# Performance work log

Measured on AMD Instinct MI355X. Metric: run time of the kernel, lower is better.

## Reference

```python
import jax, jax.numpy as jnp
import numpy as np

NQ = 12  # qubits == features of M
# (op, theta_offset_or_control, wire_or_target) mirroring TTN_node_forward
CIRCUIT = [
    ("u3", 0, 0), ("u3", 3, 1), ("cx", 0, 1),
    ("u3", 6, 2), ("u3", 9, 3), ("cx", 3, 2),
    ("u3", 12, 4), ("u3", 15, 5), ("cx", 4, 5),
    ("u3", 18, 6), ("u3", 21, 7), ("cx", 7, 6),
    ("u3", 24, 8), ("u3", 27, 9), ("cx", 8, 9),
    ("u3", 30, 10), ("u3", 33, 11), ("cx", 11, 10),
    ("u3", 36, 1), ("u3", 39, 2), ("cx", 1, 2),
    ("u3", 42, 5), ("u3", 45, 6), ("cx", 6, 5),
    ("u3", 48, 9), ("u3", 51, 10), ("cx", 10, 9),
    ("u3", 54, 2), ("u3", 57, 5), ("cx", 2, 5),
    ("u3", 60, 5), ("u3", 63, 9), ("cx", 5, 9),
    ("u3", 66, 4),
]

def _u3(theta, phi, lam):
    ct, st = jnp.cos(theta / 2), jnp.sin(theta / 2)
    r0 = jnp.stack([ct + 0j, -jnp.exp(1j * lam) * st])
    r1 = jnp.stack([jnp.exp(1j * phi) * st, jnp.exp(1j * (phi + lam)) * ct])
    return jnp.stack([r0, r1])  # [2,2] complex64

def _apply_1q(state, U, w):
    # state: (N, 2, ..., 2) with 12 qubit axes; contract U into axis w+1
    out = jnp.tensordot(U, state, axes=((1,), (w + 1,)))
    return jnp.moveaxis(out, 0, w + 1)

def _apply_cnot(state, c, t):
    c_ax, t_ax = c + 1, t + 1
    s0 = jnp.take(state, 0, axis=c_ax)
    s1 = jnp.take(state, 1, axis=c_ax)
    t_adj = t_ax - 1 if t_ax > c_ax else t_ax
    s1 = jnp.flip(s1, axis=t_adj)  # X on target (size-2 axis flip)
    return jnp.stack([s0, s1], axis=c_ax)

def _simulate(M, theta):
    # M: (N, 12) angles; product state from RY(M[:, q]) |0>
    N = M.shape[0]
    state = jnp.ones((N,), dtype=jnp.complex64)
    for q in range(NQ):
        qv = jnp.stack([jnp.cos(M[:, q] / 2), jnp.sin(M[:, q] / 2)], axis=-1)
        qv = qv.astype(jnp.complex64).reshape((N,) + (1,) * q + (2,))
        state = state[..., None] * qv  # (N, 2^(q+1) as axes)
    for op, a, b in CIRCUIT:
        if op == "u3":
            state = _apply_1q(state, _u3(theta[a], theta[a + 1], theta[a + 2]), b)
        else:
            state = _apply_cnot(state, a, b)
    p = jnp.real(state) ** 2 + jnp.imag(state) ** 2  # probabilities
    sum_axes = tuple(ax for ax in range(1, NQ + 1) if ax != 10)  # keep wire 9
    pz = p.sum(axis=sum_axes)  # (N, 2)
    return pz[:, 0] - pz[:, 1]  # <Z_9>

def setup_inputs() -> dict:
    key = jax.random.key(0)
    k1, k2, k3, k4, k5 = jax.random.split(key, 5)
    N, E = 2048, 4096
    X = jax.random.normal(k1, (N, 4), dtype=jnp.float32)
    e = jax.random.uniform(k2, (E,), dtype=jnp.float32)
    Ri = jax.random.uniform(k3, (N, E), dtype=jnp.float32)
    Ro = jax.random.uniform(k4, (N, E), dtype=jnp.float32)
    theta_learn = jax.random.uniform(k5, (69,), dtype=jnp.float32,
                                     minval=0.0, maxval=2.0 * np.pi)
    return {"X": X, "e": e, "Ri": Ri, "Ro": Ro, "theta_learn": theta_learn}

def reference(X, e, Ri, Ro, theta_learn):
    bo = jnp.einsum('ne,nd->ed', Ro, X)          # Ro^T X
    bi = jnp.einsum('ne,nd->ed', Ri, X)          # Ri^T X
    mi = jnp.einsum('ne,ed->nd', Ri * e[None, :], bo)
    mo = jnp.einsum('ne,ed->nd', Ro * e[None, :], bi)
    M = jnp.concatenate([mi, mo, X], axis=1)     # (N, 12)
    z = _simulate(M, theta_learn)
    return jnp.pi * (1.0 - z)                    # 2*pi*(1 - <Z>)/2
```

## Files before the change

kernel.cpp:

```cpp
#include <hip/hip_runtime.h>
#include <math.h>

#define N_SAMPLES 2048
#define E_EDGES   4096
#define NSPLIT    64
#define SPB       4

__global__ __launch_bounds__(256) void k_partial(const float* __restrict__ Ri,
                                                 const float* __restrict__ Ro,
                                                 const float* __restrict__ X,
                                                 float* __restrict__ pbo,
                                                 float* __restrict__ pbi) {
    __shared__ float comb[128][33];

    const int ec   = blockIdx.x;
    const int ns   = blockIdx.y;
    const int t    = threadIdx.x;
    const int col  = t & 127;
    const int half = t >> 7;
    const int v    = ec * 128 + col;

    const float4* Ri4 = reinterpret_cast<const float4*>(Ri);
    const float4* Ro4 = reinterpret_cast<const float4*>(Ro);
    const float4* X4  = reinterpret_cast<const float4*>(X);

    float abo[4][4], abi[4][4];
#pragma unroll
    for (int c = 0; c < 4; ++c)
#pragma unroll
        for (int d = 0; d < 4; ++d) { abo[c][d] = 0.f; abi[c][d] = 0.f; }

    const int n0 = ns * 32 + half * 16;
#pragma unroll 4
    for (int n = n0; n < n0 + 16; ++n) {
        float4 xv = X4[n];
        float4 ro = Ro4[(size_t)n * 1024 + v];
        float4 ri = Ri4[(size_t)n * 1024 + v];
        float xs[4]  = {xv.x, xv.y, xv.z, xv.w};
        float ros[4] = {ro.x, ro.y, ro.z, ro.w};
        float ris[4] = {ri.x, ri.y, ri.z, ri.w};
#pragma unroll
        for (int c = 0; c < 4; ++c)
#pragma unroll
            for (int d = 0; d < 4; ++d) {
                abo[c][d] += ros[c] * xs[d];
                abi[c][d] += ris[c] * xs[d];
            }
    }

    if (half) {
#pragma unroll
        for (int c = 0; c < 4; ++c)
#pragma unroll
            for (int d = 0; d < 4; ++d) {
                comb[col][c * 4 + d]      = abo[c][d];
                comb[col][16 + c * 4 + d] = abi[c][d];
            }
    }
    __syncthreads();
    if (!half) {
        float4* pbo4 = reinterpret_cast<float4*>(pbo);
        float4* pbi4 = reinterpret_cast<float4*>(pbi);
#pragma unroll
        for (int c = 0; c < 4; ++c) {
#pragma unroll
            for (int d = 0; d < 4; ++d) {
                abo[c][d] += comb[col][c * 4 + d];
                abi[c][d] += comb[col][16 + c * 4 + d];
            }
            size_t idx = (size_t)ns * E_EDGES + 4 * (size_t)v + c;
            pbo4[idx] = make_float4(abo[c][0], abo[c][1], abo[c][2], abo[c][3]);
            pbi4[idx] = make_float4(abi[c][0], abi[c][1], abi[c][2], abi[c][3]);
        }
    }
}

__global__ __launch_bounds__(256) void k_reduce(const float* __restrict__ pbo,
                                                const float* __restrict__ pbi,
                                                const float* __restrict__ ev,
                                                float* __restrict__ boT,
                                                float* __restrict__ biT) {
    const int gid = blockIdx.x * 256 + threadIdx.x;
    const int q   = gid & 3;
    const int e   = (gid >> 2) & 4095;
    const int mat = gid >> 14;
    const float4* src = reinterpret_cast<const float4*>(mat ? pbi : pbo);
    float*        dst = mat ? biT : boT;

    float s0 = 0.f, s1 = 0.f, s2 = 0.f, s3 = 0.f;
#pragma unroll 4
    for (int ns = q * 16; ns < q * 16 + 16; ++ns) {
        float4 a = src[(size_t)ns * E_EDGES + e];
        s0 += a.x; s1 += a.y; s2 += a.z; s3 += a.w;
    }
    s0 += __shfl_xor(s0, 1); s0 += __shfl_xor(s0, 2);
    s1 += __shfl_xor(s1, 1); s1 += __shfl_xor(s1, 2);
    s2 += __shfl_xor(s2, 1); s2 += __shfl_xor(s2, 2);
    s3 += __shfl_xor(s3, 1); s3 += __shfl_xor(s3, 2);
    if (q == 0) {
        const float w = ev[e];
        dst[0 * E_EDGES + e] = w * s0;
        dst[1 * E_EDGES + e] = w * s1;
        dst[2 * E_EDGES + e] = w * s2;
        dst[3 * E_EDGES + e] = w * s3;
    }
}

__global__ __launch_bounds__(256) void k_sim(const float* __restrict__ Ri,
                                             const float* __restrict__ Ro,
                                             const float* __restrict__ X,
                                             const float* __restrict__ th,
                                             const float* __restrict__ boT,
                                             const float* __restrict__ biT,
                                             float* __restrict__ out) {
    __shared__ float  redM[4][SPB][8];
    __shared__ float  R[22][9];
    __shared__ float  sM[SPB][12], cM[SPB][12];

    const int n0   = blockIdx.x * SPB;
    const int t    = threadIdx.x;
    const int lane = t & 63;
    const int wv   = t >> 6;

    if (t < 22) {
        float T = th[3 * t], P = th[3 * t + 1], L = th[3 * t + 2];
        float st, ct, sp, cp, sl, cl;
        sincosf(T, &st, &ct);
        sincosf(P, &sp, &cp);
        sincosf(L, &sl, &cl);
        R[t][0] =  cp * ct * cl - sp * sl;
        R[t][1] = -cp * ct * sl - sp * cl;
        R[t][2] =  cp * st;
        R[t][3] =  sp * ct * cl + cp * sl;
        R[t][4] = -sp * ct * sl + cp * cl;
        R[t][5] =  sp * st;
        R[t][6] = -st * cl;
        R[t][7] =  st * sl;
        R[t][8] =  ct;
    }

    float accf[SPB][8];
#pragma unroll
    for (int s = 0; s < SPB; ++s)
#pragma unroll
        for (int j = 0; j < 8; ++j) accf[s][j] = 0.f;

    const float4* Ri4s[SPB];
    const float4* Ro4s[SPB];
#pragma unroll
    for (int s = 0; s < SPB; ++s) {
        Ri4s[s] = reinterpret_cast<const float4*>(Ri + (size_t)(n0 + s) * E_EDGES);
        Ro4s[s] = reinterpret_cast<const float4*>(Ro + (size_t)(n0 + s) * E_EDGES);
    }
    const float4* BO0 = reinterpret_cast<const float4*>(boT);
    const float4* BO1 = reinterpret_cast<const float4*>(boT + E_EDGES);
    const float4* BO2 = reinterpret_cast<const float4*>(boT + 2 * E_EDGES);
    const float4* BO3 = reinterpret_cast<const float4*>(boT + 3 * E_EDGES);
    const float4* BI0 = reinterpret_cast<const float4*>(biT);
    const float4* BI1 = reinterpret_cast<const float4*>(biT + E_EDGES);
    const float4* BI2 = reinterpret_cast<const float4*>(biT + 2 * E_EDGES);
    const float4* BI3 = reinterpret_cast<const float4*>(biT + 3 * E_EDGES);

#pragma unroll
    for (int k = 0; k < 4; ++k) {
        const int v = t + 256 * k;
        const float4 o0 = BO0[v], o1 = BO1[v], o2 = BO2[v], o3 = BO3[v];
        const float4 i0 = BI0[v], i1 = BI1[v], i2 = BI2[v], i3 = BI3[v];
#pragma unroll
        for (int s = 0; s < SPB; ++s) {
            const float4 ri = Ri4s[s][v];
            const float4 ro = Ro4s[s][v];
            accf[s][0] += ri.x * o0.x + ri.y * o0.y + ri.z * o0.z + ri.w * o0.w;
            accf[s][1] += ri.x * o1.x + ri.y * o1.y + ri.z * o1.z + ri.w * o1.w;
            accf[s][2] += ri.x * o2.x + ri.y * o2.y + ri.z * o2.z + ri.w * o2.w;
            accf[s][3] += ri.x * o3.x + ri.y * o3.y + ri.z * o3.z + ri.w * o3.w;
            accf[s][4] += ro.x * i0.x + ro.y * i0.y + ro.z * i0.z + ro.w * i0.w;
            accf[s][5] += ro.x * i1.x + ro.y * i1.y + ro.z * i1.z + ro.w * i1.w;
            accf[s][6] += ro.x * i2.x + ro.y * i2.y + ro.z * i2.z + ro.w * i2.w;
            accf[s][7] += ro.x * i3.x + ro.y * i3.y + ro.z * i3.z + ro.w * i3.w;
        }
    }

#pragma unroll
    for (int off = 32; off >= 1; off >>= 1)
#pragma unroll
        for (int s = 0; s < SPB; ++s)
#pragma unroll
            for (int j = 0; j < 8; ++j)
                accf[s][j] += __shfl_xor(accf[s][j], off);
    if (lane == 0)
#pragma unroll
        for (int s = 0; s < SPB; ++s)
#pragma unroll
            for (int j = 0; j < 8; ++j) redM[wv][s][j] = accf[s][j];
    __syncthreads();

    if (t < 12 * SPB) {
        const int s = t / 12, w = t % 12;
        double Mw = (w < 8)
            ? ((double)redM[0][s][w] + (double)redM[1][s][w] +
               (double)redM[2][s][w] + (double)redM[3][s][w])
            : (double)X[(n0 + s) * 4 + (w - 8)];
        double sv, cv;
        sincos(Mw, &sv, &cv);
        sM[s][w] = (float)sv; cM[s][w] = (float)cv;
    }
    __syncthreads();

    if (t < SPB) {
        const float* sMv = sM[t];
        const float* cMv = cM[t];
        auto iz = [&](int g) -> float {
            return R[g][6] * sMv[g] + R[g][8] * cMv[g];
        };
        auto ivec = [&](int g, float& x, float& y, float& z) {
            x = R[g][0] * sMv[g] + R[g][2] * cMv[g];
            y = R[g][3] * sMv[g] + R[g][5] * cMv[g];
            z = R[g][6] * sMv[g] + R[g][8] * cMv[g];
        };
        auto rot = [&](int g, float& x, float& y, float& z) {
            float nx = R[g][0] * x + R[g][1] * y + R[g][2] * z;
            float ny = R[g][3] * x + R[g][4] * y + R[g][5] * z;
            float nz = R[g][6] * x + R[g][7] * y + R[g][8] * z;
            x = nx; y = ny; z = nz;
        };

        const float z0  = iz(0),  z3  = iz(3), z4 = iz(4);
        const float z7  = iz(7),  z8  = iz(8), z11 = iz(11);

        float x1, y1, z1;  ivec(1, x1, y1, z1);
        y1 *= z0;  z1 *= z0;          rot(12, x1, y1, z1);

        float x2, y2, z2;  ivec(2, x2, y2, z2);
        y2 *= z3;  z2 *= z3;          rot(13, x2, y2, z2);
        y2 *= z1;  z2 *= z1;          rot(18, x2, y2, z2);

        float x6, y6, z6;  ivec(6, x6, y6, z6);
        y6 *= z7;  z6 *= z7;          rot(15, x6, y6, z6);

        float x5, y5, z5;  ivec(5, x5, y5, z5);
        y5 *= z4;  z5 *= z4;          rot(14, x5, y5, z5);
        y5 *= z6;  z5 *= z6;          rot(19, x5, y5, z5);
        y5 *= z2;  z5 *= z2;          rot(20, x5, y5, z5);

        float xA, yA, zA;  ivec(10, xA, yA, zA);
        yA *= z11; zA *= z11;         rot(17, xA, yA, zA);

        float x9, y9, z9;  ivec(9, x9, y9, z9);
        y9 *= z8;  z9 *= z8;          rot(16, x9, y9, z9);
        y9 *= zA;  z9 *= zA;          rot(21, x9, y9, z9);
        z9 *= z5;

        out[n0 + t] = (float)(3.14159265358979323846 * (1.0 - (double)z9));
    }
}

extern "C" void kernel_launch(void* const* d_in, const int* in_sizes, int n_in,
                              void* d_out, int out_size, void* d_ws, size_t ws_size,
                              hipStream_t stream) {
    (void)in_sizes; (void)n_in; (void)out_size; (void)ws_size;
    const float* X  = (const float*)d_in[0];
    const float* ev = (const float*)d_in[1];
    const float* Ri = (const float*)d_in[2];
    const float* Ro = (const float*)d_in[3];
    const float* th = (const float*)d_in[4];
    float* out = (float*)d_out;

    float* pbo = (float*)d_ws;
    float* pbi = pbo + (size_t)NSPLIT * E_EDGES * 4;
    float* boT = pbi + (size_t)NSPLIT * E_EDGES * 4;
    float* biT = boT + (size_t)4 * E_EDGES;

    hipLaunchKernelGGL(k_partial, dim3(8, NSPLIT), dim3(256), 0, stream,
                       Ri, Ro, X, pbo, pbi);
    hipLaunchKernelGGL(k_reduce, dim3(128), dim3(256), 0, stream,
                       pbo, pbi, ev, boT, biT);
    hipLaunchKernelGGL(k_sim, dim3(N_SAMPLES / SPB), dim3(256), 0, stream,
                       Ri, Ro, X, th, boT, biT, out);
}
```

Before: 38.36 us.

## Double split count for partial Gram sums and use nontemporal partial stores

Splits the N dimension of the Ro^T X / Ri^T X partial products into 128 chunks instead of 64, doubling the k_partial grid to 1024 blocks to raise occupancy on the bandwidth-bound streaming pass. The reduce kernel is widened to 8 lanes per edge with an extra shuffle step and twice the blocks. Partial results are written and read with nontemporal hints to avoid polluting cache. In exchange, the partial buffers double in size, adding write and read traffic in the reduce stage.

```diff
diff --git a/kernel.cpp b/kernel.cpp
--- a/kernel.cpp
+++ b/kernel.cpp
@@ -3,8 +3,18 @@
 
 #define N_SAMPLES 2048
 #define E_EDGES   4096
-#define NSPLIT    64
+#define NSPLIT    128
 #define SPB       4
+
+typedef float f32x4 __attribute__((ext_vector_type(4)));
+
+__device__ __forceinline__ void nt_store4(float* p, float a, float b, float c, float d) {
+    f32x4 v = { a, b, c, d };
+    __builtin_nontemporal_store(v, (f32x4*)p);
+}
+__device__ __forceinline__ f32x4 nt_load4(const float* p) {
+    return __builtin_nontemporal_load((const f32x4*)p);
+}
 
 __global__ __launch_bounds__(256) void k_partial(const float* __restrict__ Ri,
                                                  const float* __restrict__ Ro,
@@ -30,9 +40,9 @@
 #pragma unroll
         for (int d = 0; d < 4; ++d) { abo[c][d] = 0.f; abi[c][d] = 0.f; }
 
-    const int n0 = ns * 32 + half * 16;
-#pragma unroll 4
-    for (int n = n0; n < n0 + 16; ++n) {
+    const int n0 = ns * 16 + half * 8;
+#pragma unroll
+    for (int n = n0; n < n0 + 8; ++n) {
         float4 xv = X4[n];
         float4 ro = Ro4[(size_t)n * 1024 + v];
         float4 ri = Ri4[(size_t)n * 1024 + v];
@@ -59,8 +69,6 @@
     }
     __syncthreads();
     if (!half) {
-        float4* pbo4 = reinterpret_cast<float4*>(pbo);
-        float4* pbi4 = reinterpret_cast<float4*>(pbi);
 #pragma unroll
         for (int c = 0; c < 4; ++c) {
 #pragma unroll
@@ -68,9 +76,9 @@
                 abo[c][d] += comb[col][c * 4 + d];
                 abi[c][d] += comb[col][16 + c * 4 + d];
             }
-            size_t idx = (size_t)ns * E_EDGES + 4 * (size_t)v + c;
-            pbo4[idx] = make_float4(abo[c][0], abo[c][1], abo[c][2], abo[c][3]);
-            pbi4[idx] = make_float4(abi[c][0], abi[c][1], abi[c][2], abi[c][3]);
+            size_t idx = 4 * ((size_t)ns * E_EDGES + 4 * (size_t)v + c);
+            nt_store4(pbo + idx, abo[c][0], abo[c][1], abo[c][2], abo[c][3]);
+            nt_store4(pbi + idx, abi[c][0], abi[c][1], abi[c][2], abi[c][3]);
         }
     }
 }
@@ -81,22 +89,22 @@
                                                 float* __restrict__ boT,
                                                 float* __restrict__ biT) {
     const int gid = blockIdx.x * 256 + threadIdx.x;
-    const int q   = gid & 3;
-    const int e   = (gid >> 2) & 4095;
-    const int mat = gid >> 14;
-    const float4* src = reinterpret_cast<const float4*>(mat ? pbi : pbo);
-    float*        dst = mat ? biT : boT;
+    const int q   = gid & 7;
+    const int e   = (gid >> 3) & 4095;
+    const int mat = gid >> 15;
+    const float* src = mat ? pbi : pbo;
+    float*       dst = mat ? biT : boT;
 
     float s0 = 0.f, s1 = 0.f, s2 = 0.f, s3 = 0.f;
 #pragma unroll 4
     for (int ns = q * 16; ns < q * 16 + 16; ++ns) {
-        float4 a = src[(size_t)ns * E_EDGES + e];
+        f32x4 a = nt_load4(src + 4 * ((size_t)ns * E_EDGES + e));
         s0 += a.x; s1 += a.y; s2 += a.z; s3 += a.w;
     }
-    s0 += __shfl_xor(s0, 1); s0 += __shfl_xor(s0, 2);
-    s1 += __shfl_xor(s1, 1); s1 += __shfl_xor(s1, 2);
-    s2 += __shfl_xor(s2, 1); s2 += __shfl_xor(s2, 2);
-    s3 += __shfl_xor(s3, 1); s3 += __shfl_xor(s3, 2);
+    s0 += __shfl_xor(s0, 1); s0 += __shfl_xor(s0, 2); s0 += __shfl_xor(s0, 4);
+    s1 += __shfl_xor(s1, 1); s1 += __shfl_xor(s1, 2); s1 += __shfl_xor(s1, 4);
+    s2 += __shfl_xor(s2, 1); s2 += __shfl_xor(s2, 2); s2 += __shfl_xor(s2, 4);
+    s3 += __shfl_xor(s3, 1); s3 += __shfl_xor(s3, 2); s3 += __shfl_xor(s3, 4);
     if (q == 0) {
         const float w = ev[e];
         dst[0 * E_EDGES + e] = w * s0;
@@ -273,7 +281,7 @@
 
     hipLaunchKernelGGL(k_partial, dim3(8, NSPLIT), dim3(256), 0, stream,
                        Ri, Ro, X, pbo, pbi);
-    hipLaunchKernelGGL(k_reduce, dim3(128), dim3(256), 0, stream,
+    hipLaunchKernelGGL(k_reduce, dim3(256), dim3(256), 0, stream,
                        pbo, pbi, ev, boT, biT);
     hipLaunchKernelGGL(k_sim, dim3(N_SAMPLES / SPB), dim3(256), 0, stream,
                        Ri, Ro, X, th, boT, biT, out);
```

Measured after the change: 60.04 us. +56.5%, slower.
